# Kernel optimization log

Hardware: AMD Instinct MI355X
Metric: run time of the kernel (lower is better)

The kernel has to match this reference:

```python
import jax, jax.numpy as jnp
import numpy as np

BS, C, C2, H, W = 8, 256, 128, 64, 64

def setup_inputs() -> dict:
    key = jax.random.key(0)
    ks = jax.random.split(key, 9)
    s = 0.05
    return {
        "appearance_1": jax.random.normal(ks[0], (BS, C2, H, W), jnp.float32),
        "appearance_2": jax.random.normal(ks[1], (BS, C2, H, W), jnp.float32),
        "motion": jax.random.normal(ks[2], (BS, C, H, W), jnp.float32),
        "Wq": jax.random.normal(ks[3], (C2, C2), jnp.float32) * s,
        "bq": jax.random.normal(ks[4], (C2,), jnp.float32) * s,
        "Wk": jax.random.normal(ks[5], (C2, C2), jnp.float32) * s,
        "bk": jax.random.normal(ks[6], (C2,), jnp.float32) * s,
        "Wv": jax.random.normal(ks[7], (C, C), jnp.float32) * s,
        "bv": jax.random.normal(ks[8], (C,), jnp.float32) * s,
    }

def reference(appearance_1, appearance_2, motion, Wq, bq, Wk, bk, Wv, bv):
    bs, c, h, w = motion.shape
    n = h * w
    a1 = appearance_1.reshape(bs, -1, n)   # [b, C2, N]
    a2 = appearance_2.reshape(bs, -1, n)   # [b, C2, N]
    m = motion.reshape(bs, c, n)           # [b, C,  N]
    # 1x1 convs == per-pixel linear projections
    q = jnp.einsum('oc,bcn->bon', Wq, a2) + bq[None, :, None]  # [b, C2, N]
    k = jnp.einsum('oc,bcn->bon', Wk, a1) + bk[None, :, None]  # [b, C2, N]
    v = jnp.einsum('oc,bcn->bon', Wv, m) + bv[None, :, None]   # [b, C,  N]
    # energy[b, i, j] = <q[:, i], k[:, j]> ; softmax over j
    energy = jnp.einsum('bci,bcj->bij', q, k)                  # [b, N, N]
    attention = jax.nn.softmax(energy, axis=-1)
    # out = V @ attention^T
    out = jnp.einsum('bcj,bij->bci', v, attention)             # [b, C, N]
    out = out.reshape(bs, c, h, w)
    fuse_out = out * motion
    return (fuse_out, out)
```

## Files before the change

### kernel.cpp

```cpp
#include <hip/hip_runtime.h>
#include <cstdint>
#include <cstddef>

#define BS   8
#define C    256
#define C2   128
#define NPIX 4096

typedef unsigned short u16;
typedef unsigned int   u32;
typedef __bf16 bf16_t;
typedef bf16_t bf16x8 __attribute__((ext_vector_type(8)));
typedef float  f32x16 __attribute__((ext_vector_type(16)));

__device__ __forceinline__ u16 f2bf(float f) {
    union { float ff; u32 i; } x; x.ff = f;
    u32 r = x.i + 0x7fffu + ((x.i >> 16) & 1u);
    return (u16)(r >> 16);
}
__device__ __forceinline__ float bf2f(u16 h) {
    union { u32 i; float f; } x; x.i = (u32)h << 16; return x.f;
}
__device__ __forceinline__ u32 pk2(u16 a, u16 b) { return (u32)a | ((u32)b << 16); }

__global__ __launch_bounds__(256)
void prep_w(const float* __restrict__ Wq, const float* __restrict__ Wk,
            const float* __restrict__ Wv,
            u16* __restrict__ qh, u16* __restrict__ ql,
            u16* __restrict__ kh, u16* __restrict__ kl,
            u16* __restrict__ vh, u16* __restrict__ vl) {
    const int z = blockIdx.y;
    const int O = (z == 2) ? C : C2;
    const int npair = O * O / 8;
    const int idx = blockIdx.x * 256 + threadIdx.x;
    if (idx >= npair) return;
    const int o  = idx & (O - 1);
    const int c8 = idx >> ((z == 2) ? 8 : 7);
    const float* src = (z == 0) ? Wq : (z == 1) ? Wk : Wv;
    u16* oh = (z == 0) ? qh : (z == 1) ? kh : vh;
    u16* ol = (z == 0) ? ql : (z == 1) ? kl : vl;
    u16 h[8], l[8];
    #pragma unroll
    for (int j = 0; j < 8; ++j) {
        const float f = src[(size_t)o * O + c8 * 8 + j];
        h[j] = f2bf(f);
        l[j] = f2bf(f - bf2f(h[j]));
    }
    *(uint4*)(oh + (size_t)idx * 8) =
        make_uint4(pk2(h[0], h[1]), pk2(h[2], h[3]), pk2(h[4], h[5]), pk2(h[6], h[7]));
    *(uint4*)(ol + (size_t)idx * 8) =
        make_uint4(pk2(l[0], l[1]), pk2(l[2], l[3]), pk2(l[4], l[5]), pk2(l[6], l[7]));
}

__global__ __launch_bounds__(256, 4)
void proj_all(const u16* __restrict__ wqh, const u16* __restrict__ wql,
              const u16* __restrict__ wkh, const u16* __restrict__ wkl,
              const u16* __restrict__ wvh, const u16* __restrict__ wvl,
              const float* __restrict__ bq, const float* __restrict__ bk,
              const float* __restrict__ bv,
              const float* __restrict__ a2, const float* __restrict__ a1,
              const float* __restrict__ motion,
              u16* __restrict__ qout, u16* __restrict__ kout,
              u16* __restrict__ vout) {
    __shared__ __align__(16) u16 Xb[16][64][8];
    const int t  = threadIdx.x;
    const int w  = t >> 6;
    const int li = t & 31;
    const int hs = (t >> 5) & 1;
    const int z  = blockIdx.z;
    const int b  = blockIdx.y;

    if (z < 2) {
        const u16* wh = z ? wkh : wqh;
        const u16* wl = z ? wkl : wql;
        const float* bias = z ? bk : bq;
        const float* x    = z ? a1 : a2;
        u16* out          = z ? kout : qout;
        const int n0 = blockIdx.x * 64;
        {
            const int sn = t & 63;
            const float* xb = x + (size_t)b * C2 * NPIX + n0 + sn;
            #pragma unroll
            for (int q = 0; q < 4; ++q) {
                const int c8 = q * 4 + w;
                union { bf16_t e[8]; uint4 u4; } cv;
                #pragma unroll
                for (int j = 0; j < 8; ++j)
                    cv.e[j] = (bf16_t)xb[(size_t)(c8 * 8 + j) * NPIX];
                *(uint4*)&Xb[c8][sn][0] = cv.u4;
            }
        }
        __syncthreads();

        f32x16 acc[2];
        #pragma unroll
        for (int nt = 0; nt < 2; ++nt)
            #pragma unroll
            for (int e = 0; e < 16; ++e) acc[nt][e] = 0.f;

        const int ob = w * 32 + li;
        #pragma unroll
        for (int ks = 0; ks < 8; ++ks) {
            const int c8 = ks * 2 + hs;
            const bf16x8 bh = *(const bf16x8*)(wh + ((size_t)c8 * C2 + ob) * 8);
            const bf16x8 bl = *(const bf16x8*)(wl + ((size_t)c8 * C2 + ob) * 8);
            #pragma unroll
            for (int nt = 0; nt < 2; ++nt) {
                const bf16x8 a = *(const bf16x8*)&Xb[c8][nt * 32 + li][0];
                acc[nt] = __builtin_amdgcn_mfma_f32_32x32x16_bf16(a, bh, acc[nt], 0, 0, 0);
                acc[nt] = __builtin_amdgcn_mfma_f32_32x32x16_bf16(a, bl, acc[nt], 0, 0, 0);
            }
        }

        const float bb = bias[ob];
        #pragma unroll
        for (int nt = 0; nt < 2; ++nt)
            #pragma unroll
            for (int r = 0; r < 16; ++r) {
                const int n = n0 + nt * 32 + (r & 3) + 8 * (r >> 2) + 4 * hs;
                out[((size_t)b * NPIX + n) * C2 + ob] = f2bf(acc[nt][r] + bb);
            }
    } else {
        u16 (*Xv)[32][8] = (u16 (*)[32][8])(&Xb[0][0][0]);
        const int n0 = blockIdx.x * 64 + (z - 2) * 32;
        {
            const int sn = t & 31;
            const int cg = t >> 5;
            const float* xb = motion + (size_t)b * C * NPIX + n0 + sn;
            #pragma unroll
            for (int r = 0; r < 4; ++r) {
                const int c8 = r * 8 + cg;
                union { bf16_t e[8]; uint4 u4; } cv;
                #pragma unroll
                for (int j = 0; j < 8; ++j)
                    cv.e[j] = (bf16_t)xb[(size_t)(c8 * 8 + j) * NPIX];
                *(uint4*)&Xv[c8][sn][0] = cv.u4;
            }
        }
        __syncthreads();

        f32x16 acc[2];
        #pragma unroll
        for (int ot = 0; ot < 2; ++ot)
            #pragma unroll
            for (int e = 0; e < 16; ++e) acc[ot][e] = 0.f;

        #pragma unroll
        for (int ks = 0; ks < 16; ++ks) {
            const int c8 = ks * 2 + hs;
            const bf16x8 xf = *(const bf16x8*)&Xv[c8][li][0];
            #pragma unroll
            for (int ot = 0; ot < 2; ++ot) {
                const int o = w * 64 + ot * 32 + li;
                const bf16x8 ah = *(const bf16x8*)(wvh + ((size_t)c8 * C + o) * 8);
                const bf16x8 al = *(const bf16x8*)(wvl + ((size_t)c8 * C + o) * 8);
                acc[ot] = __builtin_amdgcn_mfma_f32_32x32x16_bf16(ah, xf, acc[ot], 0, 0, 0);
                acc[ot] = __builtin_amdgcn_mfma_f32_32x32x16_bf16(al, xf, acc[ot], 0, 0, 0);
            }
        }

        #pragma unroll
        for (int ot = 0; ot < 2; ++ot)
            #pragma unroll
            for (int g = 0; g < 4; ++g) {
                const int orow = w * 64 + ot * 32 + 8 * g + 4 * hs;
                const float4 b4 = *(const float4*)&bv[orow];
                const size_t base = ((size_t)b * C + orow) * NPIX + n0 + li;
                vout[base]            = f2bf(acc[ot][g * 4 + 0] + b4.x);
                vout[base + NPIX]     = f2bf(acc[ot][g * 4 + 1] + b4.y);
                vout[base + 2 * NPIX] = f2bf(acc[ot][g * 4 + 2] + b4.z);
                vout[base + 3 * NPIX] = f2bf(acc[ot][g * 4 + 3] + b4.w);
            }
    }
}

struct SR { uint4 k[2]; uint4 v[4]; };

__device__ __forceinline__ void stg_load(const u16* __restrict__ kg,
                                         const u16* __restrict__ vg,
                                         int jt, int t, SR& R) {
    const u16* kp = kg + (size_t)jt * 32 * 128;
    #pragma unroll
    for (int q = 0; q < 2; ++q)
        R.k[q] = *(const uint4*)(kp + (size_t)(t + 256 * q) * 8);
    const u16* vp = vg + jt * 32 + (t & 3) * 8;
    #pragma unroll
    for (int q = 0; q < 4; ++q)
        R.v[q] = *(const uint4*)(vp + (size_t)((t >> 2) + 64 * q) * NPIX);
}

__device__ __forceinline__ void stg_write(u16* __restrict__ kb, u16* __restrict__ vb,
                                          int t, const SR& R) {
    #pragma unroll
    for (int q = 0; q < 2; ++q) {
        const int idx = t + 256 * q;
        const int row = idx >> 4;
        const int ch  = (idx & 15) ^ (row & 15);
        *(uint4*)(kb + row * 128 + ch * 8) = R.k[q];
    }
    #pragma unroll
    for (int q = 0; q < 4; ++q) {
        const int c   = (t >> 2) + 64 * q;
        const int rc  = c >> 1;
        const int q8  = (c & 1) * 8 + (t & 3) * 2;
        const int x   = rc & 15;
        const int ch0 = q8 ^ x;
        const int ch1 = (q8 + 1) ^ x;
        *(uint2*)(vb + rc * 64 + ch0 * 4) = make_uint2(R.v[q].x, R.v[q].y);
        *(uint2*)(vb + rc * 64 + ch1 * 4) = make_uint2(R.v[q].z, R.v[q].w);
    }
}

__global__ __launch_bounds__(256, 2)
void attn_mfma3(const u16* __restrict__ qt,
                const u16* __restrict__ kt,
                const u16* __restrict__ vn,
                float* __restrict__ opart0,
                float* __restrict__ opart1,
                float* __restrict__ sbuf) {
    __shared__ u16 Kb[2][32 * 128];
    __shared__ u16 Vb[2][128 * 64];

    const int t  = threadIdx.x;
    const int w  = t >> 6;
    const int li = t & 31;
    const int hs = (t >> 5) & 1;

    const int b  = blockIdx.x & 7;
    const int it = (blockIdx.x >> 3) & 31;
    const int h  = blockIdx.x >> 8;
    const int i0 = it * 128;
    const int iw = i0 + w * 32 + li;
    const int j0 = h * 2048;

    bf16x8 qf[8];
    {
        const u16* qp = qt + ((size_t)b * NPIX + iw) * C2 + hs * 8;
        #pragma unroll
        for (int ct = 0; ct < 8; ++ct) qf[ct] = *(const bf16x8*)(qp + ct * 16);
    }

    f32x16 oacc[8];
    #pragma unroll
    for (int ct = 0; ct < 8; ++ct)
        #pragma unroll
        for (int e = 0; e < 16; ++e) oacc[ct][e] = 0.f;

    const u16* ktb = kt + ((size_t)b * NPIX + j0) * C2;
    const u16* vnb = vn + (size_t)b * C * NPIX + j0;

    SR R;
    stg_load(ktb, vnb, 0, t, R);
    stg_write(&Kb[0][0], &Vb[0][0], t, R);
    stg_load(ktb, vnb, 1, t, R);
    __syncthreads();

    float ssl = 0.f;
    for (int itr = 0; itr < 64; ++itr) {
        const int cur = itr & 1;
        if (itr < 63) {
            stg_write(&Kb[cur ^ 1][0], &Vb[cur ^ 1][0], t, R);
            if (itr < 62) stg_load(ktb, vnb, itr + 2, t, R);
        }
        const u16* kb = &Kb[cur][0];
        const u16* vb = &Vb[cur][0];

        f32x16 s;
        #pragma unroll
        for (int e = 0; e < 16; ++e) s[e] = 0.f;
        {
            const int xr = li & 15;
            __builtin_amdgcn_s_setprio(1);
            #pragma unroll
            for (int ct = 0; ct < 8; ++ct) {
                const int ch = (ct * 2 + hs) ^ xr;
                const bf16x8 kf = *(const bf16x8*)(kb + li * 128 + ch * 8);
                s = __builtin_amdgcn_mfma_f32_32x32x16_bf16(kf, qf[ct], s, 0, 0, 0);
            }
            __builtin_amdgcn_s_setprio(0);
        }

        u32 pk[8];
        #pragma unroll
        for (int n = 0; n < 8; ++n) {
            const float p0 = __expf(s[2 * n]);
            const float p1 = __expf(s[2 * n + 1]);
            ssl += p0 + p1;
            union { bf16_t e[2]; u32 u; } cv;
            cv.e[0] = (bf16_t)p0;
            cv.e[1] = (bf16_t)p1;
            pk[n] = cv.u;
        }

        bf16x8 pf[2];
        #pragma unroll
        for (int seg = 0; seg < 2; ++seg) {
            const u32 A0 = pk[4 * seg + 0], A1 = pk[4 * seg + 1];
            const u32 A2 = pk[4 * seg + 2], A3 = pk[4 * seg + 3];
            const u32 own0 = hs ? A2 : A0, own1 = hs ? A3 : A1;
            const u32 snd0 = hs ? A0 : A2, snd1 = hs ? A1 : A3;
            const u32 rcv0 = (u32)__shfl_xor((int)snd0, 32, 64);
            const u32 rcv1 = (u32)__shfl_xor((int)snd1, 32, 64);
            union { u32 u[4]; bf16x8 v; } bb;
            bb.u[0] = hs ? rcv0 : own0;
            bb.u[1] = hs ? rcv1 : own1;
            bb.u[2] = hs ? own0 : rcv0;
            bb.u[3] = hs ? own1 : rcv1;
            pf[seg] = bb.v;
        }

        __builtin_amdgcn_s_setprio(1);
        #pragma unroll
        for (int ct = 0; ct < 8; ++ct) {
            const int c  = ct * 32 + li;
            const int rc = c >> 1;
            const int x  = rc & 15;
            const u16* vr = vb + rc * 64;
            const int cb = (c & 1) * 8 + hs * 2;
            #pragma unroll
            for (int seg = 0; seg < 2; ++seg) {
                const int q8  = cb + seg * 4;
                const int ch0 = q8 ^ x;
                const int ch1 = (q8 + 1) ^ x;
                union { uint2 g[2]; bf16x8 v8; } u;
                u.g[0] = *(const uint2*)(vr + ch0 * 4);
                u.g[1] = *(const uint2*)(vr + ch1 * 4);
                oacc[ct] = __builtin_amdgcn_mfma_f32_32x32x16_bf16(u.v8, pf[seg], oacc[ct], 0, 0, 0);
            }
        }
        __builtin_amdgcn_s_setprio(0);
        __syncthreads();
    }

    ssl += __shfl_xor(ssl, 32, 64);
    if (hs == 0) sbuf[((size_t)h * BS + b) * NPIX + iw] = ssl;

    float* op = h ? opart1 : opart0;
    #pragma unroll
    for (int ct = 0; ct < 8; ++ct) {
        #pragma unroll
        for (int r = 0; r < 16; ++r) {
            const int c = ct * 32 + (r & 3) + 8 * (r >> 2) + 4 * hs;
            op[((size_t)b * C + c) * NPIX + iw] = oacc[ct][r];
        }
    }
}

__global__ __launch_bounds__(256)
void attn_merge(float* __restrict__ fuse,
                float* __restrict__ outp,
                const float* __restrict__ motion,
                const float* __restrict__ sbuf) {
    const size_t idx = ((size_t)blockIdx.x * 256 + threadIdx.x) * 4;
    const int n = (int)(idx & (NPIX - 1));
    const int b = (int)(idx >> 20);
    const float4 o1 = *(const float4*)(fuse + idx);
    const float4 o2 = *(const float4*)(outp + idx);
    const float4 sa = *(const float4*)(sbuf + (size_t)b * NPIX + n);
    const float4 sb = *(const float4*)(sbuf + (size_t)(BS + b) * NPIX + n);
    float4 o;
    o.x = (o1.x + o2.x) / (sa.x + sb.x);
    o.y = (o1.y + o2.y) / (sa.y + sb.y);
    o.z = (o1.z + o2.z) / (sa.z + sb.z);
    o.w = (o1.w + o2.w) / (sa.w + sb.w);
    const float4 mv = *(const float4*)(motion + idx);
    *(float4*)(outp + idx) = o;
    *(float4*)(fuse + idx) = make_float4(o.x * mv.x, o.y * mv.y, o.z * mv.z, o.w * mv.w);
}

extern "C" void kernel_launch(void* const* d_in, const int* in_sizes, int n_in,
                              void* d_out, int out_size, void* d_ws, size_t ws_size,
                              hipStream_t stream) {
    const float* a1     = (const float*)d_in[0];
    const float* a2     = (const float*)d_in[1];
    const float* motion = (const float*)d_in[2];
    const float* Wq = (const float*)d_in[3];
    const float* bq = (const float*)d_in[4];
    const float* Wk = (const float*)d_in[5];
    const float* bk = (const float*)d_in[6];
    const float* Wv = (const float*)d_in[7];
    const float* bv = (const float*)d_in[8];

    float* outp = (float*)d_out;
    float* slot0 = outp;
    float* slot1 = outp + (size_t)BS * C * NPIX;

    u16* qws = (u16*)d_ws;
    u16* kws = qws + (size_t)BS * C2 * NPIX;
    u16* vws = kws + (size_t)BS * C2 * NPIX;
    float* sbuf = (float*)(vws + (size_t)BS * C * NPIX);
    u16* wqh = (u16*)(sbuf + (size_t)2 * BS * NPIX);
    u16* wql = wqh + C2 * C2;
    u16* wkh = wql + C2 * C2;
    u16* wkl = wkh + C2 * C2;
    u16* wvh = wkl + C2 * C2;
    u16* wvl = wvh + C * C;

    const dim3 blk(256);
    prep_w<<<dim3(32, 3), blk, 0, stream>>>(Wq, Wk, Wv, wqh, wql, wkh, wkl, wvh, wvl);
    proj_all<<<dim3(NPIX / 64, BS, 4), blk, 0, stream>>>(
        wqh, wql, wkh, wkl, wvh, wvl, bq, bk, bv, a2, a1, motion, qws, kws, vws);

    attn_mfma3<<<dim3(512), blk, 0, stream>>>(qws, kws, vws, slot0, slot1, sbuf);

    attn_merge<<<dim3((BS * C * NPIX) / 1024), blk, 0, stream>>>(
        slot0, slot1, motion, sbuf);
}
```

Before: 302.3 us.

## Fuse split-KV merge into attention kernel via atomic last-block reduction

Removes the separate merge kernel. The second of each pair of split-j attention blocks to finish is chosen with an atomic counter, and that block combines the two partial outputs, normalises them and applies the motion multiply. It also folds log2(e) into Wq and bq so the softmax can use exp2f instead of __expf. The counters are reset in prep_w. This saves a kernel launch and lets the merge overlap with other attention blocks, but the merge work now sits serially at the tail of half the blocks.

```diff
diff --git a/kernel.cpp b/kernel.cpp
--- a/kernel.cpp
+++ b/kernel.cpp
@@ -13,6 +13,8 @@
 typedef bf16_t bf16x8 __attribute__((ext_vector_type(8)));
 typedef float  f32x16 __attribute__((ext_vector_type(16)));
 
+#define RCP_LN2 1.4426950408889634f
+
 __device__ __forceinline__ u16 f2bf(float f) {
     union { float ff; u32 i; } x; x.ff = f;
     u32 r = x.i + 0x7fffu + ((x.i >> 16) & 1u);
@@ -28,7 +30,10 @@
             const float* __restrict__ Wv,
             u16* __restrict__ qh, u16* __restrict__ ql,
             u16* __restrict__ kh, u16* __restrict__ kl,
-            u16* __restrict__ vh, u16* __restrict__ vl) {
+            u16* __restrict__ vh, u16* __restrict__ vl,
+            int* __restrict__ cnt) {
+    if (blockIdx.x == 0 && blockIdx.y == 0 && threadIdx.x < BS * 32)
+        cnt[threadIdx.x] = 0;
     const int z = blockIdx.y;
     const int O = (z == 2) ? C : C2;
     const int npair = O * O / 8;
@@ -39,10 +44,11 @@
     const float* src = (z == 0) ? Wq : (z == 1) ? Wk : Wv;
     u16* oh = (z == 0) ? qh : (z == 1) ? kh : vh;
     u16* ol = (z == 0) ? ql : (z == 1) ? kl : vl;
+    const float scale = (z == 0) ? RCP_LN2 : 1.0f;
     u16 h[8], l[8];
     #pragma unroll
     for (int j = 0; j < 8; ++j) {
-        const float f = src[(size_t)o * O + c8 * 8 + j];
+        const float f = src[(size_t)o * O + c8 * 8 + j] * scale;
         h[j] = f2bf(f);
         l[j] = f2bf(f - bf2f(h[j]));
     }
@@ -112,7 +118,7 @@
             }
         }
 
-        const float bb = bias[ob];
+        const float bb = bias[ob] * (z ? 1.0f : RCP_LN2);
         #pragma unroll
         for (int nt = 0; nt < 2; ++nt)
             #pragma unroll
@@ -212,14 +218,17 @@
 }
 
 __global__ __launch_bounds__(256, 2)
-void attn_mfma3(const u16* __restrict__ qt,
+void attn_fused(const u16* __restrict__ qt,
                 const u16* __restrict__ kt,
                 const u16* __restrict__ vn,
                 float* __restrict__ opart0,
                 float* __restrict__ opart1,
-                float* __restrict__ sbuf) {
+                float* __restrict__ sbuf,
+                const float* __restrict__ motion,
+                int* __restrict__ cnt) {
     __shared__ u16 Kb[2][32 * 128];
     __shared__ u16 Vb[2][128 * 64];
+    __shared__ int loser;
 
     const int t  = threadIdx.x;
     const int w  = t >> 6;
@@ -283,8 +292,8 @@
         u32 pk[8];
         #pragma unroll
         for (int n = 0; n < 8; ++n) {
-            const float p0 = __expf(s[2 * n]);
-            const float p1 = __expf(s[2 * n + 1]);
+            const float p0 = exp2f(s[2 * n]);
+            const float p1 = exp2f(s[2 * n + 1]);
             ssl += p0 + p1;
             union { bf16_t e[2]; u32 u; } cv;
             cv.e[0] = (bf16_t)p0;
@@ -344,28 +353,41 @@
             op[((size_t)b * C + c) * NPIX + iw] = oacc[ct][r];
         }
     }
-}
-
-__global__ __launch_bounds__(256)
-void attn_merge(float* __restrict__ fuse,
-                float* __restrict__ outp,
-                const float* __restrict__ motion,
-                const float* __restrict__ sbuf) {
-    const size_t idx = ((size_t)blockIdx.x * 256 + threadIdx.x) * 4;
-    const int n = (int)(idx & (NPIX - 1));
-    const int b = (int)(idx >> 20);
-    const float4 o1 = *(const float4*)(fuse + idx);
-    const float4 o2 = *(const float4*)(outp + idx);
-    const float4 sa = *(const float4*)(sbuf + (size_t)b * NPIX + n);
-    const float4 sb = *(const float4*)(sbuf + (size_t)(BS + b) * NPIX + n);
-    float4 o;
-    o.x = (o1.x + o2.x) / (sa.x + sb.x);
-    o.y = (o1.y + o2.y) / (sa.y + sb.y);
-    o.z = (o1.z + o2.z) / (sa.z + sb.z);
-    o.w = (o1.w + o2.w) / (sa.w + sb.w);
-    const float4 mv = *(const float4*)(motion + idx);
-    *(float4*)(outp + idx) = o;
-    *(float4*)(fuse + idx) = make_float4(o.x * mv.x, o.y * mv.y, o.z * mv.z, o.w * mv.w);
+
+    __syncthreads();
+    if (t == 0) {
+        __threadfence();
+        const int old = atomicAdd(&cnt[(b << 5) | it], 1);
+        loser = (old == 1);
+    }
+    __syncthreads();
+    if (!loser) return;
+    __threadfence();
+
+    const int ti = t & 31, tc = t >> 5;
+    const float4 va = *(const float4*)(sbuf + (size_t)b * NPIX + i0 + ti * 4);
+    const float4 vb4 = *(const float4*)(sbuf + ((size_t)BS + b) * NPIX + i0 + ti * 4);
+    float4 rd;
+    rd.x = 1.f / (va.x + vb4.x);
+    rd.y = 1.f / (va.y + vb4.y);
+    rd.z = 1.f / (va.z + vb4.z);
+    rd.w = 1.f / (va.w + vb4.w);
+    #pragma unroll 4
+    for (int cc = 0; cc < 32; ++cc) {
+        const int c = cc * 8 + tc;
+        const size_t base = ((size_t)b * C + c) * NPIX + i0 + ti * 4;
+        const float4 p0 = *(const float4*)(opart0 + base);
+        const float4 p1 = *(const float4*)(opart1 + base);
+        const float4 mv = *(const float4*)(motion + base);
+        float4 o;
+        o.x = (p0.x + p1.x) * rd.x;
+        o.y = (p0.y + p1.y) * rd.y;
+        o.z = (p0.z + p1.z) * rd.z;
+        o.w = (p0.w + p1.w) * rd.w;
+        *(float4*)(opart1 + base) = o;
+        *(float4*)(opart0 + base) = make_float4(o.x * mv.x, o.y * mv.y,
+                                                o.z * mv.z, o.w * mv.w);
+    }
 }
 
 extern "C" void kernel_launch(void* const* d_in, const int* in_sizes, int n_in,
@@ -395,14 +417,14 @@
     u16* wkl = wkh + C2 * C2;
     u16* wvh = wkl + C2 * C2;
     u16* wvl = wvh + C * C;
+    int* cnt = (int*)(wvl + C * C);
 
     const dim3 blk(256);
-    prep_w<<<dim3(32, 3), blk, 0, stream>>>(Wq, Wk, Wv, wqh, wql, wkh, wkl, wvh, wvl);
+    prep_w<<<dim3(32, 3), blk, 0, stream>>>(
+        Wq, Wk, Wv, wqh, wql, wkh, wkl, wvh, wvl, cnt);
     proj_all<<<dim3(NPIX / 64, BS, 4), blk, 0, stream>>>(
         wqh, wql, wkh, wkl, wvh, wvl, bq, bk, bv, a2, a1, motion, qws, kws, vws);
 
-    attn_mfma3<<<dim3(512), blk, 0, stream>>>(qws, kws, vws, slot0, slot1, sbuf);
-
-    attn_merge<<<dim3((BS * C * NPIX) / 1024), blk, 0, stream>>>(
-        slot0, slot1, motion, sbuf);
-}
+    attn_fused<<<dim3(512), blk, 0, stream>>>(
+        qws, kws, vws, slot0, slot1, sbuf, motion, cnt);
+}
```

New measurement: 366.6 us. 1.21x slower.
